# Kernel tuning notes

Hardware: AMD Instinct MI355X
Metric: run time of the kernel (lower is better)

## Reference

```python
import jax, jax.numpy as jnp
import numpy as np
import math

IN_F = 2048
INTER_F = 8192
OUT_F = 2048
STRIPE = 256
N_STRIPES = INTER_F // STRIPE
EPS = 1e-7
BETA = 0.99
STEPS = 1000.0
THRESH_LR_SCALE = 1.0 * math.sqrt(IN_F)


def setup_inputs() -> dict:
    key = jax.random.key(0)
    ks = jax.random.split(key, 8)
    x = jax.random.normal(ks[0], (2, 1024, IN_F), dtype=jnp.float32)
    gate_weight = jax.random.normal(ks[1], (IN_F, INTER_F), dtype=jnp.float32) / math.sqrt(IN_F)
    gate_bias = jnp.zeros((INTER_F,), dtype=jnp.float32)
    # thresholds ~ threshold_init scale so the mask is non-trivially sparse
    gate_thresholds = jax.random.uniform(ks[2], (N_STRIPES, IN_F), dtype=jnp.float32) * (0.1 / THRESH_LR_SCALE) * 20.0
    med = jax.random.normal(ks[3], (IN_F,), dtype=jnp.float32) * 0.01
    aad = jax.random.uniform(ks[4], (IN_F,), dtype=jnp.float32) + 0.5
    up_weight = jax.random.normal(ks[5], (IN_F, INTER_F), dtype=jnp.float32) * 0.02
    up_bias = jnp.zeros((INTER_F,), dtype=jnp.float32)
    down_weight = jax.random.normal(ks[6], (OUT_F, INTER_F), dtype=jnp.float32) / math.sqrt(INTER_F)
    down_bias = jnp.zeros((OUT_F,), dtype=jnp.float32)
    return dict(x=x, gate_weight=gate_weight, gate_bias=gate_bias,
                gate_thresholds=gate_thresholds, med=med, aad=aad,
                up_weight=up_weight, up_bias=up_bias,
                down_weight=down_weight, down_bias=down_bias)


def _cwic_linear(xf, weight, bias, thresholds, med, aad):
    # eval-mode CWICLinear. xf: [T, I]
    debiaser = 1.0 / (EPS + (1.0 - BETA ** STEPS))
    mu = med * debiaser                                   # [I]
    std = aad * debiaser / math.sqrt(2.0 * math.pi)      # [I]
    thr = thresholds * std[None, :] * THRESH_LR_SCALE     # [N, I]
    xd = xf - mu[None, :]                                 # [T, I]
    mask = (jnp.abs(xd)[:, None, :] > thr[None]).astype(xf.dtype)  # [T, N, I]
    xm = xd[:, None, :] * mask + mu[None, None, :]        # [T, N, I]
    w = weight.T.reshape(N_STRIPES, STRIPE, IN_F)          # [N, S, I]
    y = jnp.einsum('nsi,tni->tns', w, xm).reshape(-1, INTER_F) + bias[None, :]
    active = STRIPE * mask.reshape(xf.shape[0], -1).sum(axis=-1)  # [T]
    dense = jnp.full_like(active, STRIPE * N_STRIPES * IN_F)
    return y, dense, active


def reference(x, gate_weight, gate_bias, gate_thresholds, med, aad,
              up_weight, up_bias, down_weight, down_bias):
    B, T, I = x.shape
    xf = x.reshape(-1, I)
    g, dense, active = _cwic_linear(xf, gate_weight, gate_bias, gate_thresholds, med, aad)
    up = xf @ up_weight + up_bias[None, :]                 # Conv1D: x @ W + b
    h = jax.nn.silu(g) * up                                # [BT, inter]
    y = h @ down_weight.T + down_bias[None, :]             # nn.Linear
    return (y.reshape(B, T, OUT_F), dense.reshape(B, T), active.reshape(B, T))
```

## Files before the change

### kernel.cpp

```cpp
#include <hip/hip_runtime.h>
#include <math.h>
#include <stdint.h>

typedef __bf16 bf16_t;
typedef __bf16 bf16x8 __attribute__((ext_vector_type(8)));
typedef __bf16 bf16x4 __attribute__((ext_vector_type(4)));
typedef float f32x4 __attribute__((ext_vector_type(4)));
typedef short s16x8 __attribute__((ext_vector_type(8)));

#define TOKS 2048
#define INF 2048
#define JNF 8192
#define ONF 2048


template <int ROWS, int NT>
__device__ __forceinline__ void stage_async_t(const bf16_t* __restrict__ src, size_t ld,
                                              bf16_t* lds, int tid) {
  constexpr int IT = ROWS * 8 / NT;
#pragma unroll
  for (int r = 0; r < IT; ++r) {
    int c = r * NT + tid;
    int row = c >> 3;
    int kq = (c & 7) ^ (row & 7);
    const bf16_t* g = src + (size_t)row * ld + kq * 8;
    bf16_t* l = lds + (size_t)(r * NT + (tid & ~63)) * 8;
    __builtin_amdgcn_global_load_lds((const __attribute__((address_space(1))) void*)g,
                                     (__attribute__((address_space(3))) void*)l,
                                     16, 0, 0);
  }
}

__device__ __forceinline__ bf16x8 frag_ld64(const bf16_t* lds, int row, int kq) {
  int slot = kq ^ (row & 7);
  return *(const bf16x8*)&lds[row * 64 + slot * 8];
}


__global__ __launch_bounds__(256) void prep_mu_thr(
    const float* __restrict__ med, const float* __restrict__ aad,
    const float* __restrict__ gth, float debiaser,
    float* __restrict__ mu, float* __restrict__ thr, bf16_t* __restrict__ thrb) {
  int gid = blockIdx.x * 256 + threadIdx.x;
  if (gid < INF) mu[gid] = med[gid] * debiaser;
  int i = gid & (INF - 1);
  float stdv = aad[i] * debiaser / 2.5066282746310002f;
  float tv = gth[gid] * stdv * 45.254833995939045f;
  thr[gid] = tv;
  thrb[gid] = (bf16_t)tv;
}

__global__ __launch_bounds__(256) void prep_x_count(
    const float* __restrict__ x, const float* __restrict__ mu,
    const float* __restrict__ thr,
    bf16_t* __restrict__ xb, bf16_t* __restrict__ xdb,
    float* __restrict__ dense, float* __restrict__ active) {
  int t = blockIdx.x;
  int tid = threadIdx.x;
  int i0 = tid * 8;
  const float* xrow = x + (size_t)t * INF;
  f32x4 x0 = *(const f32x4*)&xrow[i0];
  f32x4 x1 = *(const f32x4*)&xrow[i0 + 4];
  f32x4 m0 = *(const f32x4*)&mu[i0];
  f32x4 m1 = *(const f32x4*)&mu[i0 + 4];
  f32x4 d0 = x0 - m0, d1 = x1 - m1;
  bf16x8 ox, od;
  ox[0] = (bf16_t)x0[0]; ox[1] = (bf16_t)x0[1]; ox[2] = (bf16_t)x0[2]; ox[3] = (bf16_t)x0[3];
  ox[4] = (bf16_t)x1[0]; ox[5] = (bf16_t)x1[1]; ox[6] = (bf16_t)x1[2]; ox[7] = (bf16_t)x1[3];
  od[0] = (bf16_t)d0[0]; od[1] = (bf16_t)d0[1]; od[2] = (bf16_t)d0[2]; od[3] = (bf16_t)d0[3];
  od[4] = (bf16_t)d1[0]; od[5] = (bf16_t)d1[1]; od[6] = (bf16_t)d1[2]; od[7] = (bf16_t)d1[3];
  *(bf16x8*)&xb[(size_t)t * INF + i0] = ox;
  *(bf16x8*)&xdb[(size_t)t * INF + i0] = od;
  f32x4 a0, a1;
  a0[0] = fabsf(d0[0]); a0[1] = fabsf(d0[1]); a0[2] = fabsf(d0[2]); a0[3] = fabsf(d0[3]);
  a1[0] = fabsf(d1[0]); a1[1] = fabsf(d1[1]); a1[2] = fabsf(d1[2]); a1[3] = fabsf(d1[3]);
  int cnt = 0;
#pragma unroll 4
  for (int n = 0; n < 32; ++n) {
    f32x4 t0 = *(const f32x4*)&thr[(n << 11) + i0];
    f32x4 t1 = *(const f32x4*)&thr[(n << 11) + i0 + 4];
    cnt += (a0[0] > t0[0]) + (a0[1] > t0[1]) + (a0[2] > t0[2]) + (a0[3] > t0[3]);
    cnt += (a1[0] > t1[0]) + (a1[1] > t1[1]) + (a1[2] > t1[2]) + (a1[3] > t1[3]);
  }
  for (int off = 32; off; off >>= 1) cnt += __shfl_down(cnt, off);
  __shared__ int red[4];
  int wv = tid >> 6;
  if ((tid & 63) == 0) red[wv] = cnt;
  __syncthreads();
  if (tid == 0) {
    int tot = red[0] + red[1] + red[2] + red[3];
    active[t] = 256.0f * (float)tot;
    dense[t] = 16777216.0f;
  }
}

__global__ __launch_bounds__(256) void transpose_cast_dual(
    const float* __restrict__ src0, bf16_t* __restrict__ dst0,
    const float* __restrict__ src1, bf16_t* __restrict__ dst1) {
  const float* src = blockIdx.z ? src1 : src0;
  bf16_t* dst = blockIdx.z ? dst1 : dst0;
  __shared__ float tile[32][33];
  int j0 = blockIdx.x * 32;
  int i0 = blockIdx.y * 32;
  int r = threadIdx.x >> 3;
  int c = (threadIdx.x & 7) * 4;
  f32x4 v = *(const f32x4*)&src[(i0 + r) * JNF + j0 + c];
  tile[r][c] = v[0]; tile[r][c + 1] = v[1]; tile[r][c + 2] = v[2]; tile[r][c + 3] = v[3];
  __syncthreads();
  bf16x4 o;
  o[0] = (bf16_t)tile[c + 0][r];
  o[1] = (bf16_t)tile[c + 1][r];
  o[2] = (bf16_t)tile[c + 2][r];
  o[3] = (bf16_t)tile[c + 3][r];
  *(bf16x4*)&dst[(j0 + r) * INF + i0 + c] = o;
}

__global__ __launch_bounds__(256) void cast_bf16(
    const float* __restrict__ src, bf16_t* __restrict__ dst) {
  int idx = (blockIdx.x * 256 + threadIdx.x) * 8;
  f32x4 a = *(const f32x4*)&src[idx];
  f32x4 b = *(const f32x4*)&src[idx + 4];
  bf16x8 o;
  o[0] = (bf16_t)a[0]; o[1] = (bf16_t)a[1]; o[2] = (bf16_t)a[2]; o[3] = (bf16_t)a[3];
  o[4] = (bf16_t)b[0]; o[5] = (bf16_t)b[1]; o[6] = (bf16_t)b[2]; o[7] = (bf16_t)b[3];
  *(bf16x8*)&dst[idx] = o;
}

__global__ __launch_bounds__(256) void c_from_gwT(
    const bf16_t* __restrict__ gwT, const float* __restrict__ mu,
    const float* __restrict__ gb, float* __restrict__ c) {
  int j = blockIdx.x * 4 + (threadIdx.x >> 6);
  int lane = threadIdx.x & 63;
  float s = 0.f;
#pragma unroll
  for (int it = 0; it < 4; ++it) {
    int i = it * 512 + lane * 8;
    bf16x8 w = *(const bf16x8*)&gwT[(size_t)j * INF + i];
    f32x4 m0 = *(const f32x4*)&mu[i];
    f32x4 m1 = *(const f32x4*)&mu[i + 4];
    s += (float)w[0] * m0[0] + (float)w[1] * m0[1] + (float)w[2] * m0[2] + (float)w[3] * m0[3];
    s += (float)w[4] * m1[0] + (float)w[5] * m1[1] + (float)w[6] * m1[2] + (float)w[7] * m1[3];
  }
  for (int off = 32; off; off >>= 1) s += __shfl_down(s, off);
  if (lane == 0) c[j] = gb[j] + s;
}


template <int MODE>
__global__ __launch_bounds__(512) void gemm256(
    const bf16_t* __restrict__ Ag, const bf16_t* __restrict__ Bg,
    const bf16_t* __restrict__ thrv, const float* __restrict__ cvec,
    const bf16_t* __restrict__ gmat, bf16_t* __restrict__ outb,
    float* __restrict__ outf) {
  constexpr int NTILES = 32;
  constexpr size_t LD = (MODE == 1) ? (size_t)JNF : (size_t)INF;
  __shared__ bf16_t Al[2][256 * 64];
  __shared__ bf16_t Bl[2][256 * 64];
  int tid = threadIdx.x;
  int lane = tid & 63;
  int wv = tid >> 6;
  int wm = wv >> 2;
  int wn = wv & 3;
  int m16 = lane & 15, q = lane >> 4;
  int t0 = blockIdx.y * 256;
  int j0 = blockIdx.x * 256;
  int kbeg = (MODE == 1) ? blockIdx.z * 2048 : 0;
  const bf16_t* Arow = Ag + (size_t)t0 * LD + kbeg;
  const bf16_t* Brow = Bg + (size_t)j0 * LD + kbeg;
  const bf16_t* Tn = (MODE == 2) ? thrv + (size_t)blockIdx.x * INF : (const bf16_t*)nullptr;
  const s16x8 ABS = {0x7FFF, 0x7FFF, 0x7FFF, 0x7FFF, 0x7FFF, 0x7FFF, 0x7FFF, 0x7FFF};

  f32x4 acc[8][4] = {};

  stage_async_t<256, 512>(Brow, LD, Bl[0], tid);
  if constexpr (MODE == 2) {
    s16x8 av0[4], tv0[4];
#pragma unroll
    for (int r2 = 0; r2 < 4; ++r2) {
      int ch = r2 * 512 + tid;
      int row = ch >> 3;
      int kq = (ch & 7) ^ (row & 7);
      av0[r2] = *(const s16x8*)&Arow[(size_t)row * LD + kq * 8];
      tv0[r2] = *(const s16x8*)&Tn[kq * 8];
    }
#pragma unroll
    for (int r2 = 0; r2 < 4; ++r2) {
      int ch = r2 * 512 + tid;
      int row = ch >> 3;
      int sl = ch & 7;
      s16x8 m = (s16x8)((tv0[r2] - (av0[r2] & ABS)) >> 15);
      *(s16x8*)&Al[0][row * 64 + sl * 8] = av0[r2] & m;
    }
  } else {
    stage_async_t<256, 512>(Arow, LD, Al[0], tid);
  }
  asm volatile("s_waitcnt vmcnt(0) lgkmcnt(0)" ::: "memory");
  __builtin_amdgcn_s_barrier();

  for (int u = 0; u < NTILES; ++u) {
    int c = u & 1;
    const bf16_t* Ab = Al[c];
    const bf16_t* Bb = Bl[c];
    bf16x8 bfr[4][2];
    s16x8 av[4], tv[4];
#pragma unroll
    for (int p = 0; p < 4; ++p) {
      if (p == 0) {
        if (u + 1 < NTILES) {
          stage_async_t<256, 512>(Brow + (u + 1) * 64, LD, Bl[c ^ 1], tid);
          if constexpr (MODE == 2) {
            int k0 = (u + 1) * 64;
#pragma unroll
            for (int r2 = 0; r2 < 4; ++r2) {
              int ch = r2 * 512 + tid;
              int row = ch >> 3;
              int kq = (ch & 7) ^ (row & 7);
              av[r2] = *(const s16x8*)&Arow[(size_t)row * LD + k0 + kq * 8];
              tv[r2] = *(const s16x8*)&Tn[k0 + kq * 8];
            }
          } else {
            stage_async_t<256, 512>(Arow + (u + 1) * 64, LD, Al[c ^ 1], tid);
          }
        }
#pragma unroll
        for (int ni = 0; ni < 4; ++ni)
#pragma unroll
          for (int ks = 0; ks < 2; ++ks)
            bfr[ni][ks] = frag_ld64(Bb, wn * 64 + ni * 16 + m16, ks * 4 + q);
      }
      bf16x8 af[2][2];
#pragma unroll
      for (int mi2 = 0; mi2 < 2; ++mi2)
#pragma unroll
        for (int ks = 0; ks < 2; ++ks)
          af[mi2][ks] = frag_ld64(Ab, wm * 128 + (p * 2 + mi2) * 16 + m16, ks * 4 + q);
      if constexpr (MODE == 2) {
        if (p == 2 && u + 1 < NTILES) {
#pragma unroll
          for (int r2 = 0; r2 < 4; ++r2) {
            int ch = r2 * 512 + tid;
            int row = ch >> 3;
            int sl = ch & 7;
            s16x8 m = (s16x8)((tv[r2] - (av[r2] & ABS)) >> 15);
            *(s16x8*)&Al[c ^ 1][row * 64 + sl * 8] = av[r2] & m;
          }
        }
      }
      __builtin_amdgcn_s_barrier();
      __builtin_amdgcn_s_setprio(1);
#pragma unroll
      for (int mi2 = 0; mi2 < 2; ++mi2)
#pragma unroll
        for (int ni = 0; ni < 4; ++ni)
#pragma unroll
          for (int ks = 0; ks < 2; ++ks)
            acc[p * 2 + mi2][ni] = __builtin_amdgcn_mfma_f32_16x16x32_bf16(
                af[mi2][ks], bfr[ni][ks], acc[p * 2 + mi2][ni], 0, 0, 0);
      __builtin_amdgcn_s_setprio(0);
      if (p < 3) __builtin_amdgcn_s_barrier();
    }
    asm volatile("s_waitcnt vmcnt(0) lgkmcnt(0)" ::: "memory");
    __builtin_amdgcn_s_barrier();
  }

  int cb = j0 + wn * 64;
  int rb = t0 + wm * 128;
  if constexpr (MODE == 1) {
    float* dst = outf + (size_t)blockIdx.z * ((size_t)TOKS * ONF);
#pragma unroll
    for (int mi = 0; mi < 8; ++mi)
#pragma unroll
      for (int ni = 0; ni < 4; ++ni) {
        int col = cb + ni * 16 + m16;
#pragma unroll
        for (int r = 0; r < 4; ++r) {
          int row = rb + mi * 16 + q * 4 + r;
          dst[(size_t)row * ONF + col] = acc[mi][ni][r];
        }
      }
  } else if constexpr (MODE == 0) {
#pragma unroll
    for (int mi = 0; mi < 8; ++mi)
#pragma unroll
      for (int ni = 0; ni < 4; ++ni) {
        int col = cb + ni * 16 + m16;
        float bias = cvec[col];
#pragma unroll
        for (int r = 0; r < 4; ++r) {
          int row = rb + mi * 16 + q * 4 + r;
          float upv = acc[mi][ni][r] + bias;
          float gv = (float)gmat[(size_t)row * JNF + col];
          float hv = (gv / (1.f + expf(-gv))) * upv;
          outb[(size_t)row * JNF + col] = (bf16_t)hv;
        }
      }
  } else {
#pragma unroll
    for (int mi = 0; mi < 8; ++mi)
#pragma unroll
      for (int ni = 0; ni < 4; ++ni) {
        int col = cb + ni * 16 + m16;
        float cadd = cvec[col];
#pragma unroll
        for (int r = 0; r < 4; ++r) {
          int row = rb + mi * 16 + q * 4 + r;
          outb[(size_t)row * JNF + col] = (bf16_t)(acc[mi][ni][r] + cadd);
        }
      }
  }
}

__global__ __launch_bounds__(256) void down_reduce(
    const float* __restrict__ part, const float* __restrict__ db,
    float* __restrict__ y) {
  int idx = (blockIdx.x * 256 + threadIdx.x) * 4;
  f32x4 a = *(const f32x4*)&part[idx];
  f32x4 b = *(const f32x4*)&part[idx + 4194304];
  f32x4 c = *(const f32x4*)&part[idx + 2 * 4194304];
  f32x4 d = *(const f32x4*)&part[idx + 3 * 4194304];
  f32x4 bias = *(const f32x4*)&db[idx & (ONF - 1)];
  *(f32x4*)&y[idx] = a + b + c + d + bias;
}


extern "C" void kernel_launch(void* const* d_in, const int* in_sizes, int n_in,
                              void* d_out, int out_size, void* d_ws, size_t ws_size,
                              hipStream_t stream) {
  (void)in_sizes; (void)n_in; (void)out_size; (void)ws_size;
  const float* x   = (const float*)d_in[0];
  const float* gw  = (const float*)d_in[1];
  const float* gb  = (const float*)d_in[2];
  const float* gth = (const float*)d_in[3];
  const float* med = (const float*)d_in[4];
  const float* aad = (const float*)d_in[5];
  const float* uw  = (const float*)d_in[6];
  const float* ub  = (const float*)d_in[7];
  const float* dw  = (const float*)d_in[8];
  const float* db  = (const float*)d_in[9];

  float* out = (float*)d_out;
  float* y = out;
  float* dense = out + 4194304;
  float* active = dense + 2048;

  char* ws = (char*)d_ws;
  float*  mu   = (float*)(ws + 0);
  float*  thr  = (float*)(ws + 8192);
  bf16_t* thrb = (bf16_t*)(ws + 270336);
  float*  cj   = (float*)(ws + 401408);
  bf16_t* xb   = (bf16_t*)(ws + 434176);
  bf16_t* xdb  = (bf16_t*)(ws + 8822784);
  bf16_t* gwT  = (bf16_t*)(ws + 17211392);
  bf16_t* upT  = (bf16_t*)(ws + 50765824);
  bf16_t* dwb  = (bf16_t*)(ws + 84320256);
  bf16_t* hb   = (bf16_t*)(ws + 117874688);
  float*  part = (float*)(ws + 151429120);
  bf16_t* gb16 = (bf16_t*)part;

  float debiaser = (float)(1.0 / (1e-7 + (1.0 - pow(0.99, 1000.0))));

  prep_mu_thr<<<256, 256, 0, stream>>>(med, aad, gth, debiaser, mu, thr, thrb);
  prep_x_count<<<2048, 256, 0, stream>>>(x, mu, thr, xb, xdb, dense, active);
  transpose_cast_dual<<<dim3(256, 64, 2), 256, 0, stream>>>(gw, gwT, uw, upT);
  cast_bf16<<<8192, 256, 0, stream>>>(dw, dwb);
  c_from_gwT<<<2048, 256, 0, stream>>>(gwT, mu, gb, cj);
  gemm256<2><<<dim3(32, 8), 512, 0, stream>>>(xdb, gwT, thrb, cj, nullptr, gb16, nullptr);
  gemm256<0><<<dim3(32, 8), 512, 0, stream>>>(xb, upT, nullptr, ub, gb16, hb, nullptr);
  gemm256<1><<<dim3(8, 8, 4), 512, 0, stream>>>(hb, dwb, nullptr, nullptr, nullptr, nullptr, part);
  down_reduce<<<4096, 256, 0, stream>>>(part, db, y);
}
```

Measured before the change: 570.1 us.

## Restructure GEMM main loop into finer-grained half-tile prefetch pipeline

Replaces the double-buffered K loop, which issued one whole 256x64 tile prefetch at the start of each iteration and then waited on all of it, with a manually unrolled loop over two K-tiles per iteration. Global-to-LDS loads for A and B are split into 128-row halves and spread across the MFMA phases. Partial vmcnt waits replace full drains so loads stay in flight while MFMAs run. This risks fragile waitcnt counts and races on the LDS buffers if the counts or barriers are wrong.

```diff
diff --git a/kernel.cpp b/kernel.cpp
--- a/kernel.cpp
+++ b/kernel.cpp
@@ -13,18 +13,20 @@
 #define JNF 8192
 #define ONF 2048
 
-
-template <int ROWS, int NT>
-__device__ __forceinline__ void stage_async_t(const bf16_t* __restrict__ src, size_t ld,
-                                              bf16_t* lds, int tid) {
-  constexpr int IT = ROWS * 8 / NT;
-#pragma unroll
-  for (int r = 0; r < IT; ++r) {
-    int c = r * NT + tid;
+#define VMW(N) asm volatile("s_waitcnt vmcnt(" #N ")" ::: "memory")
+#define LGKM0 asm volatile("s_waitcnt lgkmcnt(0)" ::: "memory")
+#define BAR __builtin_amdgcn_s_barrier()
+
+
+__device__ __forceinline__ void stage_half(const bf16_t* __restrict__ src, size_t ld,
+                                           bf16_t* lds, int tid) {
+#pragma unroll
+  for (int r = 0; r < 2; ++r) {
+    int c = r * 512 + tid;
     int row = c >> 3;
     int kq = (c & 7) ^ (row & 7);
     const bf16_t* g = src + (size_t)row * ld + kq * 8;
-    bf16_t* l = lds + (size_t)(r * NT + (tid & ~63)) * 8;
+    bf16_t* l = lds + (size_t)(r * 512 + (tid & ~63)) * 8;
     __builtin_amdgcn_global_load_lds((const __attribute__((address_space(1))) void*)g,
                                      (__attribute__((address_space(3))) void*)l,
                                      16, 0, 0);
@@ -34,6 +36,67 @@
 __device__ __forceinline__ bf16x8 frag_ld64(const bf16_t* lds, int row, int kq) {
   int slot = kq ^ (row & 7);
   return *(const bf16x8*)&lds[row * 64 + slot * 8];
+}
+
+__device__ __forceinline__ void ds_bf(const bf16_t* B, int wn, int m16, int q,
+                                      bf16x8 (&bfr)[4][2]) {
+#pragma unroll
+  for (int ni = 0; ni < 4; ++ni)
+#pragma unroll
+    for (int ks = 0; ks < 2; ++ks)
+      bfr[ni][ks] = frag_ld64(B, wn * 64 + ni * 16 + m16, ks * 4 + q);
+}
+
+template <int P>
+__device__ __forceinline__ void ds_af(const bf16_t* A, int wm, int m16, int q,
+                                      bf16x8 (&af)[2][2]) {
+#pragma unroll
+  for (int mi2 = 0; mi2 < 2; ++mi2)
+#pragma unroll
+    for (int ks = 0; ks < 2; ++ks)
+      af[mi2][ks] = frag_ld64(A, wm * 128 + P * 32 + mi2 * 16 + m16, ks * 4 + q);
+}
+
+template <int P>
+__device__ __forceinline__ void mfma_ph(f32x4 (&acc)[8][4], const bf16x8 (&af)[2][2],
+                                        const bf16x8 (&bfr)[4][2]) {
+  __builtin_amdgcn_s_barrier();
+  __builtin_amdgcn_s_setprio(1);
+#pragma unroll
+  for (int mi2 = 0; mi2 < 2; ++mi2)
+#pragma unroll
+    for (int ni = 0; ni < 4; ++ni)
+#pragma unroll
+      for (int ks = 0; ks < 2; ++ks)
+        acc[P * 2 + mi2][ni] = __builtin_amdgcn_mfma_f32_16x16x32_bf16(
+            af[mi2][ks], bfr[ni][ks], acc[P * 2 + mi2][ni], 0, 0, 0);
+  __builtin_amdgcn_s_setprio(0);
+}
+
+__device__ __forceinline__ void loadA_half(const bf16_t* __restrict__ Arow, size_t ld,
+                                           const bf16_t* __restrict__ Tn, int k0, int half,
+                                           int tid, s16x8 (&av)[2], s16x8 (&tv)[2]) {
+#pragma unroll
+  for (int r = 0; r < 2; ++r) {
+    int c = r * 512 + tid;
+    int lrow = c >> 3;
+    int kq = (c & 7) ^ (lrow & 7);
+    av[r] = *(const s16x8*)&Arow[(size_t)(half * 128 + lrow) * ld + k0 + kq * 8];
+    tv[r] = *(const s16x8*)&Tn[k0 + kq * 8];
+  }
+}
+
+__device__ __forceinline__ void writeA_half(bf16_t* halfbase, int tid,
+                                            const s16x8 (&av)[2], const s16x8 (&tv)[2]) {
+  const s16x8 ABS = {0x7FFF, 0x7FFF, 0x7FFF, 0x7FFF, 0x7FFF, 0x7FFF, 0x7FFF, 0x7FFF};
+#pragma unroll
+  for (int r = 0; r < 2; ++r) {
+    int c = r * 512 + tid;
+    int lrow = c >> 3;
+    int sl = c & 7;
+    s16x8 m = (s16x8)((tv[r] - (av[r] & ABS)) >> 15);
+    *(s16x8*)&halfbase[lrow * 64 + sl * 8] = av[r] & m;
+  }
 }
 
 
@@ -152,10 +215,12 @@
     const bf16_t* __restrict__ thrv, const float* __restrict__ cvec,
     const bf16_t* __restrict__ gmat, bf16_t* __restrict__ outb,
     float* __restrict__ outf) {
-  constexpr int NTILES = 32;
   constexpr size_t LD = (MODE == 1) ? (size_t)JNF : (size_t)INF;
-  __shared__ bf16_t Al[2][256 * 64];
-  __shared__ bf16_t Bl[2][256 * 64];
+  constexpr int NIT = 16;
+  __shared__ bf16_t Als[2][256 * 64];
+  __shared__ bf16_t Bls[2][256 * 64];
+  bf16_t* Als0 = Als[0]; bf16_t* Als1 = Als[1];
+  bf16_t* Bls0 = Bls[0]; bf16_t* Bls1 = Bls[1];
   int tid = threadIdx.x;
   int lane = tid & 63;
   int wv = tid >> 6;
@@ -168,99 +233,111 @@
   const bf16_t* Arow = Ag + (size_t)t0 * LD + kbeg;
   const bf16_t* Brow = Bg + (size_t)j0 * LD + kbeg;
   const bf16_t* Tn = (MODE == 2) ? thrv + (size_t)blockIdx.x * INF : (const bf16_t*)nullptr;
-  const s16x8 ABS = {0x7FFF, 0x7FFF, 0x7FFF, 0x7FFF, 0x7FFF, 0x7FFF, 0x7FFF, 0x7FFF};
 
   f32x4 acc[8][4] = {};
-
-  stage_async_t<256, 512>(Brow, LD, Bl[0], tid);
+  bf16x8 bfr[4][2];
+  bf16x8 af[2][2];
+  s16x8 avA0[2], tvA0[2], avA1[2], tvA1[2];
+
   if constexpr (MODE == 2) {
-    s16x8 av0[4], tv0[4];
-#pragma unroll
-    for (int r2 = 0; r2 < 4; ++r2) {
-      int ch = r2 * 512 + tid;
-      int row = ch >> 3;
-      int kq = (ch & 7) ^ (row & 7);
-      av0[r2] = *(const s16x8*)&Arow[(size_t)row * LD + kq * 8];
-      tv0[r2] = *(const s16x8*)&Tn[kq * 8];
-    }
-#pragma unroll
-    for (int r2 = 0; r2 < 4; ++r2) {
-      int ch = r2 * 512 + tid;
-      int row = ch >> 3;
-      int sl = ch & 7;
-      s16x8 m = (s16x8)((tv0[r2] - (av0[r2] & ABS)) >> 15);
-      *(s16x8*)&Al[0][row * 64 + sl * 8] = av0[r2] & m;
-    }
+    loadA_half(Arow, LD, Tn, 0, 0, tid, avA0, tvA0);
+    loadA_half(Arow, LD, Tn, 0, 1, tid, avA1, tvA1);
+    VMW(0);
+    writeA_half(Als0, tid, avA0, tvA0);
+    writeA_half(Als0 + 128 * 64, tid, avA1, tvA1);
+    LGKM0;
+    stage_half(Brow, LD, Bls0, tid);
+    stage_half(Brow + (size_t)128 * LD, LD, Bls0 + 128 * 64, tid);
+    loadA_half(Arow, LD, Tn, 64, 0, tid, avA0, tvA0);
+    stage_half(Brow + 64, LD, Bls1, tid);
+    loadA_half(Arow, LD, Tn, 64, 1, tid, avA1, tvA1);
+    stage_half(Brow + (size_t)128 * LD + 64, LD, Bls1 + 128 * 64, tid);
+    VMW(12);
   } else {
-    stage_async_t<256, 512>(Arow, LD, Al[0], tid);
-  }
-  asm volatile("s_waitcnt vmcnt(0) lgkmcnt(0)" ::: "memory");
-  __builtin_amdgcn_s_barrier();
-
-  for (int u = 0; u < NTILES; ++u) {
-    int c = u & 1;
-    const bf16_t* Ab = Al[c];
-    const bf16_t* Bb = Bl[c];
-    bf16x8 bfr[4][2];
-    s16x8 av[4], tv[4];
-#pragma unroll
-    for (int p = 0; p < 4; ++p) {
-      if (p == 0) {
-        if (u + 1 < NTILES) {
-          stage_async_t<256, 512>(Brow + (u + 1) * 64, LD, Bl[c ^ 1], tid);
-          if constexpr (MODE == 2) {
-            int k0 = (u + 1) * 64;
-#pragma unroll
-            for (int r2 = 0; r2 < 4; ++r2) {
-              int ch = r2 * 512 + tid;
-              int row = ch >> 3;
-              int kq = (ch & 7) ^ (row & 7);
-              av[r2] = *(const s16x8*)&Arow[(size_t)row * LD + k0 + kq * 8];
-              tv[r2] = *(const s16x8*)&Tn[k0 + kq * 8];
-            }
-          } else {
-            stage_async_t<256, 512>(Arow + (u + 1) * 64, LD, Al[c ^ 1], tid);
-          }
-        }
-#pragma unroll
-        for (int ni = 0; ni < 4; ++ni)
-#pragma unroll
-          for (int ks = 0; ks < 2; ++ks)
-            bfr[ni][ks] = frag_ld64(Bb, wn * 64 + ni * 16 + m16, ks * 4 + q);
-      }
-      bf16x8 af[2][2];
-#pragma unroll
-      for (int mi2 = 0; mi2 < 2; ++mi2)
-#pragma unroll
-        for (int ks = 0; ks < 2; ++ks)
-          af[mi2][ks] = frag_ld64(Ab, wm * 128 + (p * 2 + mi2) * 16 + m16, ks * 4 + q);
+    stage_half(Brow, LD, Bls0, tid);
+    stage_half(Brow + (size_t)128 * LD, LD, Bls0 + 128 * 64, tid);
+    stage_half(Arow, LD, Als0, tid);
+    stage_half(Arow + (size_t)128 * LD, LD, Als0 + 128 * 64, tid);
+    stage_half(Brow + 64, LD, Bls1, tid);
+    stage_half(Brow + (size_t)128 * LD + 64, LD, Bls1 + 128 * 64, tid);
+    VMW(4);
+  }
+  BAR;
+
+  for (int i = 0; i < NIT; ++i) {
+    const bool S = (i < NIT - 1);
+    const int kb = i * 128;
+    ds_bf(Bls0, wn, m16, q, bfr);
+    ds_af<0>(Als0, wm, m16, q, af);
+    if constexpr (MODE == 2) {
+      VMW(8);
+      writeA_half(Als1, tid, avA0, tvA0);
+      LGKM0;
+    } else {
+      stage_half(Arow + kb + 64, LD, Als1, tid);
+    }
+    mfma_ph<0>(acc, af, bfr); BAR;
+    ds_af<1>(Als0, wm, m16, q, af);
+    if constexpr (MODE == 2) {
+      VMW(2);
+      writeA_half(Als1 + 128 * 64, tid, avA1, tvA1);
+      LGKM0;
+      if (S) {
+        stage_half(Brow + kb + 128, LD, Bls0, tid);
+        loadA_half(Arow, LD, Tn, kb + 128, 0, tid, avA0, tvA0);
+      }
+    } else {
+      stage_half(Arow + (size_t)128 * LD + kb + 64, LD, Als1 + 128 * 64, tid);
+      if (S) stage_half(Brow + kb + 128, LD, Bls0, tid);
+    }
+    mfma_ph<1>(acc, af, bfr); BAR;
+    ds_af<2>(Als0, wm, m16, q, af);
+    if (S) {
+      if constexpr (MODE == 2) loadA_half(Arow, LD, Tn, kb + 128, 1, tid, avA1, tvA1);
+      stage_half(Brow + (size_t)128 * LD + kb + 128, LD, Bls0 + 128 * 64, tid);
+    }
+    mfma_ph<2>(acc, af, bfr); BAR;
+    ds_af<3>(Als0, wm, m16, q, af);
+    mfma_ph<3>(acc, af, bfr);
+    if (S) { if constexpr (MODE == 2) { VMW(12); } else { VMW(4); } }
+    else   { VMW(0); }
+    BAR;
+    ds_bf(Bls1, wn, m16, q, bfr);
+    ds_af<0>(Als1, wm, m16, q, af);
+    if (S) {
       if constexpr (MODE == 2) {
-        if (p == 2 && u + 1 < NTILES) {
-#pragma unroll
-          for (int r2 = 0; r2 < 4; ++r2) {
-            int ch = r2 * 512 + tid;
-            int row = ch >> 3;
-            int sl = ch & 7;
-            s16x8 m = (s16x8)((tv[r2] - (av[r2] & ABS)) >> 15);
-            *(s16x8*)&Al[c ^ 1][row * 64 + sl * 8] = av[r2] & m;
-          }
-        }
-      }
-      __builtin_amdgcn_s_barrier();
-      __builtin_amdgcn_s_setprio(1);
-#pragma unroll
-      for (int mi2 = 0; mi2 < 2; ++mi2)
-#pragma unroll
-        for (int ni = 0; ni < 4; ++ni)
-#pragma unroll
-          for (int ks = 0; ks < 2; ++ks)
-            acc[p * 2 + mi2][ni] = __builtin_amdgcn_mfma_f32_16x16x32_bf16(
-                af[mi2][ks], bfr[ni][ks], acc[p * 2 + mi2][ni], 0, 0, 0);
-      __builtin_amdgcn_s_setprio(0);
-      if (p < 3) __builtin_amdgcn_s_barrier();
-    }
-    asm volatile("s_waitcnt vmcnt(0) lgkmcnt(0)" ::: "memory");
-    __builtin_amdgcn_s_barrier();
+        VMW(6);
+        writeA_half(Als0, tid, avA0, tvA0);
+        LGKM0;
+      } else {
+        stage_half(Arow + kb + 128, LD, Als0, tid);
+      }
+    }
+    mfma_ph<4>(acc, af, bfr); BAR;
+    ds_af<1>(Als1, wm, m16, q, af);
+    if (S) {
+      if constexpr (MODE == 2) {
+        loadA_half(Arow, LD, Tn, kb + 192, 0, tid, avA0, tvA0);
+        VMW(6);
+        writeA_half(Als0 + 128 * 64, tid, avA1, tvA1);
+        LGKM0;
+      } else {
+        stage_half(Arow + (size_t)128 * LD + kb + 128, LD, Als0 + 128 * 64, tid);
+      }
+    }
+    mfma_ph<5>(acc, af, bfr); BAR;
+    ds_af<2>(Als1, wm, m16, q, af);
+    if (S) {
+      stage_half(Brow + kb + 192, LD, Bls1, tid);
+      if constexpr (MODE == 2) loadA_half(Arow, LD, Tn, kb + 192, 1, tid, avA1, tvA1);
+    }
+    mfma_ph<6>(acc, af, bfr); BAR;
+    ds_af<3>(Als1, wm, m16, q, af);
+    if (S) stage_half(Brow + (size_t)128 * LD + kb + 192, LD, Bls1 + 128 * 64, tid);
+    mfma_ph<7>(acc, af, bfr);
+    if (S) { if constexpr (MODE == 2) { VMW(12); } else { VMW(4); } }
+    else   { VMW(0); }
+    BAR;
   }
 
   int cb = j0 + wn * 64;
```

After: 482.0 us. 15.5% less time.
